# Kernel tuning notes

Hardware: AMD Instinct MI355X
Metric: run time of the kernel (lower is better)

The kernel has to match this reference:

```python
import jax, jax.numpy as jnp
import numpy as np

N_HEADS = 32
N_KV_HEADS = 8
HEAD_DIM = 128
ROPE_BASE = 10000.0
NEG_INF = -1e9


def rope(x, base=ROPE_BASE, offset=0):
    # x: [B, H, L, d]; 'traditional' RoPE with the module's rotation formula.
    d = x.shape[-1]
    t = jnp.arange(x.shape[2], dtype=jnp.float32) + offset
    freqs = base ** (-jnp.arange(0, d, 2, dtype=jnp.float32) / d)  # [d/2]
    ang = t[:, None] * freqs[None, :]                              # [L, d/2]
    cos, sin = jnp.cos(ang), jnp.sin(ang)
    x1, x2 = x[..., 0::2], x[..., 1::2]
    out = jnp.stack([x1 * cos + x2 * sin, x1 * sin - x2 * cos], axis=-1)
    return out.reshape(x.shape)


def setup_inputs() -> dict:
    key = jax.random.key(0)
    ks = jax.random.split(key, 5)
    B, L, D = 2, 2048, 4096
    x = jax.random.normal(ks[0], (B, L, D), dtype=jnp.float32)
    wq = jax.random.normal(ks[1], (D, N_HEADS * HEAD_DIM), dtype=jnp.float32) * 0.02
    wk = jax.random.normal(ks[2], (D, N_KV_HEADS * HEAD_DIM), dtype=jnp.float32) * 0.02
    wv = jax.random.normal(ks[3], (D, N_KV_HEADS * HEAD_DIM), dtype=jnp.float32) * 0.02
    wo = jax.random.normal(ks[4], (N_HEADS * HEAD_DIM, D), dtype=jnp.float32) * 0.02
    # causal additive mask [L, L]
    mask = jnp.where(jnp.tril(jnp.ones((L, L), dtype=bool)), 0.0, NEG_INF).astype(jnp.float32)
    return {"x": x, "mask": mask, "wq": wq, "wk": wk, "wv": wv, "wo": wo}


def reference(x, mask, wq, wk, wv, wo):
    B, L, D = x.shape
    scale = HEAD_DIM ** -0.5
    q = (x @ wq).reshape(B, L, N_HEADS, HEAD_DIM).transpose(0, 2, 1, 3)     # [B,H,L,d]
    k = (x @ wk).reshape(B, L, N_KV_HEADS, HEAD_DIM).transpose(0, 2, 1, 3)  # [B,Hk,L,d]
    v = (x @ wv).reshape(B, L, N_KV_HEADS, HEAD_DIM).transpose(0, 2, 1, 3)
    rep = N_HEADS // N_KV_HEADS
    k = jnp.repeat(k, rep, axis=1)  # [B,H,L,d]  (physical GQA repeat, as in source)
    v = jnp.repeat(v, rep, axis=1)
    q = rope(q)
    k = rope(k)
    scores = jnp.einsum("bhqd,bhkd->bhqk", q * scale, k) + mask  # [B,H,L,L]
    probs = jax.nn.softmax(scores.astype(jnp.float32), axis=-1).astype(scores.dtype)
    out = jnp.einsum("bhqk,bhkd->bhqd", probs, v)
    out = out.transpose(0, 2, 1, 3).reshape(B, L, N_HEADS * HEAD_DIM)
    return out @ wo, (k, v)
```

## Files before the change

### kernel.cpp

```cpp
#include <hip/hip_runtime.h>

typedef unsigned short u16;
typedef unsigned int u32;
typedef float f32x4 __attribute__((ext_vector_type(4)));
typedef __bf16 bf16x8 __attribute__((ext_vector_type(8)));

#define DEV __device__ __forceinline__

DEV u16 f2b(float f) {
    union { float f; u32 u; } v; v.f = f;
    u32 r = v.u + 0x7fffu + ((v.u >> 16) & 1u);
    return (u16)(r >> 16);
}
DEV float b2f(u16 b) {
    union { u32 u; float f; } v; v.u = ((u32)b) << 16;
    return v.f;
}

DEV void gload16(const void* g, void* l) {
    __builtin_amdgcn_global_load_lds((const __attribute__((address_space(1))) void*)g,
                                     (__attribute__((address_space(3))) void*)l, 16, 0, 0);
}

DEV f32x4 mfma16(bf16x8 a, bf16x8 b, f32x4 c) {
    return __builtin_amdgcn_mfma_f32_16x16x32_bf16(a, b, c, 0, 0, 0);
}

__global__ __launch_bounds__(256) void convx_kernel(const float* __restrict__ in,
                                                    u16* __restrict__ out) {
    size_t i = ((size_t)blockIdx.x * 256 + threadIdx.x) * 4;
    float4 v = *(const float4*)(in + i);
    ushort4 o; o.x = f2b(v.x); o.y = f2b(v.y); o.z = f2b(v.z); o.w = f2b(v.w);
    *(ushort4*)(out + i) = o;
}

__global__ __launch_bounds__(256) void tconv_kernel(const float* __restrict__ in,
                                                    u16* __restrict__ out, int K, int N) {
    __shared__ float tile[64][65];
    int t = threadIdx.x;
    int n0 = blockIdx.x * 64, k0 = blockIdx.y * 64;
    int r = t >> 4, c4 = (t & 15) * 4;
#pragma unroll
    for (int i = 0; i < 4; ++i) {
        float4 v = *(const float4*)(in + (size_t)(k0 + i * 16 + r) * N + n0 + c4);
        tile[i * 16 + r][c4 + 0] = v.x; tile[i * 16 + r][c4 + 1] = v.y;
        tile[i * 16 + r][c4 + 2] = v.z; tile[i * 16 + r][c4 + 3] = v.w;
    }
    __syncthreads();
#pragma unroll
    for (int i = 0; i < 4; ++i) {
        int nn = i * 16 + r;
        ushort4 o;
        o.x = f2b(tile[c4 + 0][nn]); o.y = f2b(tile[c4 + 1][nn]);
        o.z = f2b(tile[c4 + 2][nn]); o.w = f2b(tile[c4 + 3][nn]);
        *(ushort4*)(out + (size_t)(n0 + nn) * K + k0 + c4) = o;
    }
}

template <bool F32OUT>
__global__ __launch_bounds__(512, 2) void gemm256_kernel(const u16* __restrict__ A,
                                                         const u16* __restrict__ Bt,
                                                         u16* __restrict__ Cb,
                                                         float* __restrict__ Cf,
                                                         int M, int N, int K, int gy) {
    __shared__ __align__(16) u16 Asb[2][2][128 * 64];
    __shared__ __align__(16) u16 Bsb[2][2][128 * 64];
    (void)M;
    int t = threadIdx.x;
    int lane = t & 63, w = t >> 6;
    int wrM = w >> 2, wcN = w & 3;
    int lr = lane & 15, hi = lane >> 4;
    int wg = blockIdx.x;
    int swz = (wg & 7) * ((int)gridDim.x >> 3) + (wg >> 3);
    int bx = swz / gy, by = swz % gy;
    int m0 = by * 256, n0 = bx * 256;
    int nk = K >> 6;

    auto stageA = [&](int X, int h) {
        const u16* src = A + (size_t)(m0 + h * 128) * K + X * 64;
        char* dst = (char*)&Asb[X & 1][h][0];
#pragma unroll
        for (int it = 0; it < 2; ++it) {
            int c = it * 512 + t;
            int row = c >> 3;
            int col8 = ((c & 7) ^ (row & 7)) << 3;
            gload16(src + (size_t)row * K + col8, dst + (it * 512 + (t & ~63)) * 16);
        }
    };
    auto stageB = [&](int X, int h) {
        const u16* src = Bt + (size_t)(n0 + h * 128) * K + X * 64;
        char* dst = (char*)&Bsb[X & 1][h][0];
#pragma unroll
        for (int it = 0; it < 2; ++it) {
            int c = it * 512 + t;
            int row = c >> 3;
            int col8 = ((c & 7) ^ (row & 7)) << 3;
            gload16(src + (size_t)row * K + col8, dst + (it * 512 + (t & ~63)) * 16);
        }
    };

    stageA(0, 0); stageA(0, 1); stageB(0, 0); stageB(0, 1);
    stageA(1, 0); stageA(1, 1); stageB(1, 0);
    asm volatile("s_waitcnt vmcnt(6)" ::: "memory");
    __builtin_amdgcn_s_barrier();

    f32x4 acc[8][4] = {};
    for (int kt = 0; kt < nk; ++kt) {
        __builtin_amdgcn_sched_barrier(0);
        int p = kt & 1;
        const char* Ah = (const char*)&Asb[p][wrM][0];
        const char* Bh = (const char*)&Bsb[p][wcN >> 1][0];
        bool s1 = (kt + 1 < nk), s2 = (kt + 2 < nk);
        bf16x8 a[8][2], bb[2][2];

#pragma unroll
        for (int mf = 0; mf < 4; ++mf)
#pragma unroll
            for (int ks = 0; ks < 2; ++ks) {
                int row = mf * 16 + lr;
                int byt = (row * 128 + ks * 64 + hi * 16) ^ ((row & 7) << 4);
                a[mf][ks] = *(const bf16x8*)(Ah + byt);
            }
#pragma unroll
        for (int nf = 0; nf < 2; ++nf)
#pragma unroll
            for (int ks = 0; ks < 2; ++ks) {
                int row = (wcN & 1) * 64 + nf * 16 + lr;
                int byt = (row * 128 + ks * 64 + hi * 16) ^ ((row & 7) << 4);
                bb[nf][ks] = *(const bf16x8*)(Bh + byt);
            }
        if (s1) stageB(kt + 1, 1);
        __builtin_amdgcn_s_barrier();
        __builtin_amdgcn_s_setprio(1);
#pragma unroll
        for (int mf = 0; mf < 4; ++mf)
#pragma unroll
            for (int nf = 0; nf < 2; ++nf)
#pragma unroll
                for (int ks = 0; ks < 2; ++ks)
                    acc[mf][nf] = mfma16(a[mf][ks], bb[nf][ks], acc[mf][nf]);
        __builtin_amdgcn_s_setprio(0);
        __builtin_amdgcn_s_barrier();

#pragma unroll
        for (int mf = 4; mf < 8; ++mf)
#pragma unroll
            for (int ks = 0; ks < 2; ++ks) {
                int row = mf * 16 + lr;
                int byt = (row * 128 + ks * 64 + hi * 16) ^ ((row & 7) << 4);
                a[mf][ks] = *(const bf16x8*)(Ah + byt);
            }
        __builtin_amdgcn_s_barrier();
        __builtin_amdgcn_s_setprio(1);
#pragma unroll
        for (int mf = 4; mf < 8; ++mf)
#pragma unroll
            for (int nf = 0; nf < 2; ++nf)
#pragma unroll
                for (int ks = 0; ks < 2; ++ks)
                    acc[mf][nf] = mfma16(a[mf][ks], bb[nf][ks], acc[mf][nf]);
        __builtin_amdgcn_s_setprio(0);
        __builtin_amdgcn_s_barrier();

#pragma unroll
        for (int nf = 0; nf < 2; ++nf)
#pragma unroll
            for (int ks = 0; ks < 2; ++ks) {
                int row = (wcN & 1) * 64 + (nf + 2) * 16 + lr;
                int byt = (row * 128 + ks * 64 + hi * 16) ^ ((row & 7) << 4);
                bb[nf][ks] = *(const bf16x8*)(Bh + byt);
            }
        if (s2) { stageA(kt + 2, 0); stageA(kt + 2, 1); }
        __builtin_amdgcn_s_barrier();
        __builtin_amdgcn_s_setprio(1);
#pragma unroll
        for (int mf = 4; mf < 8; ++mf)
#pragma unroll
            for (int nf = 0; nf < 2; ++nf)
#pragma unroll
                for (int ks = 0; ks < 2; ++ks)
                    acc[mf][nf + 2] = mfma16(a[mf][ks], bb[nf][ks], acc[mf][nf + 2]);
        __builtin_amdgcn_s_setprio(0);
        __builtin_amdgcn_s_barrier();

        if (s2) stageB(kt + 2, 0);
        __builtin_amdgcn_s_barrier();
        __builtin_amdgcn_s_setprio(1);
#pragma unroll
        for (int mf = 0; mf < 4; ++mf)
#pragma unroll
            for (int nf = 0; nf < 2; ++nf)
#pragma unroll
                for (int ks = 0; ks < 2; ++ks)
                    acc[mf][nf + 2] = mfma16(a[mf][ks], bb[nf][ks], acc[mf][nf + 2]);
        __builtin_amdgcn_s_setprio(0);
        if (s1) {
            if (s2) asm volatile("s_waitcnt vmcnt(6)" ::: "memory");
            else    asm volatile("s_waitcnt vmcnt(0)" ::: "memory");
        }
        __builtin_amdgcn_s_barrier();
    }

#pragma unroll
    for (int mf = 0; mf < 8; ++mf)
#pragma unroll
        for (int nf = 0; nf < 4; ++nf)
#pragma unroll
            for (int r = 0; r < 4; ++r) {
                int m = m0 + wrM * 128 + mf * 16 + hi * 4 + r;
                int n = n0 + wcN * 64 + nf * 16 + lr;
                if (F32OUT) Cf[(size_t)m * N + n] = acc[mf][nf][r];
                else        Cb[(size_t)m * N + n] = f2b(acc[mf][nf][r]);
            }
}

__global__ __launch_bounds__(256) void rope_kernel(u16* __restrict__ qkv,
                                                   float* __restrict__ outk) {
    int row = blockIdx.y;
    int p = blockIdx.x * 256 + threadIdx.x;
    int b = row >> 11, l = row & 2047;
    float freq = exp2f((float)(p & 63) * -0.2076205059304601f);
    float sv, cv; sincosf((float)l * freq, &sv, &cv);
    if (p < 2048) {
        int h = p >> 6, i = p & 63;
        size_t idx = (size_t)row * 6144 + h * 128 + 2 * i;
        u32 pr = *(const u32*)(qkv + idx);
        float x1 = b2f((u16)(pr & 0xffff)), x2 = b2f((u16)(pr >> 16));
        float o1 = x1 * cv + x2 * sv, o2 = x1 * sv - x2 * cv;
        *(u32*)(qkv + idx) = (u32)f2b(o1) | ((u32)f2b(o2) << 16);
    } else {
        int kvh = (p >> 6) - 32, i = p & 63;
        size_t idx = (size_t)row * 6144 + 4096 + kvh * 128 + 2 * i;
        u32 pr = *(const u32*)(qkv + idx);
        float x1 = b2f((u16)(pr & 0xffff)), x2 = b2f((u16)(pr >> 16));
        float o1 = x1 * cv + x2 * sv, o2 = x1 * sv - x2 * cv;
        *(u32*)(qkv + idx) = (u32)f2b(o1) | ((u32)f2b(o2) << 16);
#pragma unroll
        for (int r = 0; r < 4; ++r) {
            float2 o; o.x = o1; o.y = o2;
            *(float2*)(outk + ((size_t)((b * 32 + kvh * 4 + r) * 2048) + l) * 128 + 2 * i) = o;
        }
    }
}

__global__ __launch_bounds__(256) void vtrans_kernel(const u16* __restrict__ qkv,
                                                     u16* __restrict__ vt,
                                                     float* __restrict__ outv) {
    __shared__ u16 tile[64][65];
    int t = threadIdx.x;
    int l0 = blockIdx.x * 64, d0 = blockIdx.y * 64;
    int z = blockIdx.z, b = z >> 3, kvh = z & 7;
    int r = t >> 4, c4 = (t & 15) * 4;
#pragma unroll
    for (int i = 0; i < 4; ++i) {
        int l = l0 + i * 16 + r;
        ushort4 v = *(const ushort4*)(qkv + (size_t)(b * 2048 + l) * 6144 + 5120 + kvh * 128 + d0 + c4);
        tile[i * 16 + r][c4 + 0] = v.x; tile[i * 16 + r][c4 + 1] = v.y;
        tile[i * 16 + r][c4 + 2] = v.z; tile[i * 16 + r][c4 + 3] = v.w;
        float4 f; f.x = b2f(v.x); f.y = b2f(v.y); f.z = b2f(v.z); f.w = b2f(v.w);
#pragma unroll
        for (int rr = 0; rr < 4; ++rr)
            *(float4*)(outv + ((size_t)((b * 32 + kvh * 4 + rr) * 2048) + l) * 128 + d0 + c4) = f;
    }
    __syncthreads();
#pragma unroll
    for (int i = 0; i < 4; ++i) {
        int dn = i * 16 + r;
        ushort4 o;
        o.x = tile[c4 + 0][dn]; o.y = tile[c4 + 1][dn];
        o.z = tile[c4 + 2][dn]; o.w = tile[c4 + 3][dn];
        *(ushort4*)(vt + (size_t)((b * 8 + kvh) * 128 + d0 + dn) * 2048 + l0 + c4) = o;
    }
}

__global__ __launch_bounds__(256) void attn_kernel(const u16* __restrict__ qkv,
                                                   const u16* __restrict__ vt,
                                                   u16* __restrict__ ab) {
    __shared__ __align__(16) u16 Kbuf[2][64 * 128];
    __shared__ __align__(16) u16 Vbuf[2][128 * 64];
    __shared__ __align__(16) u16 Ps[4][16 * 64];
    int t = threadIdx.x, lane = t & 63, w = t >> 6;
    int lr = lane & 15, hi = lane >> 4;
    int h = blockIdx.y, b = blockIdx.z, kvh = h >> 2;

    const u16* kbase = qkv + (size_t)(b * 2048) * 6144 + 4096 + kvh * 128;
    const u16* vtbase = vt + (size_t)((b * 8 + kvh) * 128) * 2048;

    auto stageKV = [&](int k0, int buf) {
#pragma unroll
        for (int i = 0; i < 4; ++i) {
            int c = i * 256 + t;
            int row = c >> 4;
            int col8 = ((c & 15) ^ (row & 7)) << 3;
            gload16(kbase + (size_t)(k0 + row) * 6144 + col8,
                    (char*)Kbuf[buf] + (i * 256 + (t & ~63)) * 16);
        }
#pragma unroll
        for (int i = 0; i < 4; ++i) {
            int c = i * 256 + t;
            int row = c >> 3;
            int col8 = ((c & 7) ^ (row & 7)) << 3;
            gload16(vtbase + (size_t)row * 2048 + k0 + col8,
                    (char*)Vbuf[buf] + (i * 256 + (t & ~63)) * 16);
        }
    };

    auto process = [&](int qblk) {
        int q0 = qblk * 64;
        int qr = w * 16 + lr;
        bf16x8 qf[4];
#pragma unroll
        for (int kki = 0; kki < 4; ++kki)
            qf[kki] = *(const bf16x8*)(qkv + (size_t)(b * 2048 + q0 + qr) * 6144 + h * 128 +
                                       kki * 32 + 8 * hi);
        f32x4 acc[8] = {};
        float mrun[4], lrun[4];
#pragma unroll
        for (int r = 0; r < 4; ++r) { mrun[r] = -1e30f; lrun[r] = 0.f; }

        int nt = qblk + 1;
        stageKV(0, 0);
        __syncthreads();
        int cur = 0;
        for (int kt = 0; kt < nt; ++kt) {
            if (kt + 1 < nt) stageKV((kt + 1) * 64, cur ^ 1);
            __builtin_amdgcn_sched_barrier(0);

            const u16* Ks = Kbuf[cur];
            const u16* Vs = Vbuf[cur];
            f32x4 s[4] = {};
            __builtin_amdgcn_s_setprio(1);
#pragma unroll
            for (int kki = 0; kki < 4; ++kki) {
                bf16x8 kf[4];
#pragma unroll
                for (int fc = 0; fc < 4; ++fc) {
                    int kvr = fc * 16 + lr;
                    int byt = (kvr * 256 + (kki * 32 + 8 * hi) * 2) ^ ((kvr & 7) << 4);
                    kf[fc] = *(const bf16x8*)((const char*)Ks + byt);
                }
#pragma unroll
                for (int fc = 0; fc < 4; ++fc) s[fc] = mfma16(qf[kki], kf[fc], s[fc]);
            }
            __builtin_amdgcn_s_setprio(0);
            const float SC = 0.08838834764831845f;
            int diag = (kt == nt - 1);
#pragma unroll
            for (int fc = 0; fc < 4; ++fc)
#pragma unroll
                for (int r = 0; r < 4; ++r) {
                    float v = s[fc][r] * SC;
                    if (diag && (fc * 16 + lr) > (w * 16 + hi * 4 + r)) v = -1e30f;
                    s[fc][r] = v;
                }
            float fr[4];
#pragma unroll
            for (int r = 0; r < 4; ++r) {
                float v = fmaxf(fmaxf(s[0][r], s[1][r]), fmaxf(s[2][r], s[3][r]));
                v = fmaxf(v, __shfl_xor(v, 1)); v = fmaxf(v, __shfl_xor(v, 2));
                v = fmaxf(v, __shfl_xor(v, 4)); v = fmaxf(v, __shfl_xor(v, 8));
                float mn = fmaxf(mrun[r], v);
                fr[r] = __expf(mrun[r] - mn);
                mrun[r] = mn;
            }
#pragma unroll
            for (int fc = 0; fc < 4; ++fc)
#pragma unroll
                for (int r = 0; r < 4; ++r) s[fc][r] = __expf(s[fc][r] - mrun[r]);
#pragma unroll
            for (int r = 0; r < 4; ++r) {
                float v = s[0][r] + s[1][r] + s[2][r] + s[3][r];
                v += __shfl_xor(v, 1); v += __shfl_xor(v, 2);
                v += __shfl_xor(v, 4); v += __shfl_xor(v, 8);
                lrun[r] = lrun[r] * fr[r] + v;
            }
#pragma unroll
            for (int dhf = 0; dhf < 8; ++dhf)
#pragma unroll
                for (int r = 0; r < 4; ++r) acc[dhf][r] *= fr[r];
            u16* Pw = Ps[w];
#pragma unroll
            for (int fc = 0; fc < 4; ++fc)
#pragma unroll
                for (int r = 0; r < 4; ++r) {
                    int prow = hi * 4 + r, pcol = fc * 16 + lr;
                    int byt = (prow * 128 + pcol * 2) ^ ((prow & 7) << 4);
                    *(u16*)((char*)Pw + byt) = f2b(s[fc][r]);
                }
            asm volatile("s_waitcnt lgkmcnt(0)" ::: "memory");
            __builtin_amdgcn_s_setprio(1);
#pragma unroll
            for (int kk2 = 0; kk2 < 2; ++kk2) {
                int bytp = (lr * 128 + (kk2 * 32 + 8 * hi) * 2) ^ ((lr & 7) << 4);
                bf16x8 pf = *(const bf16x8*)((const char*)Pw + bytp);
#pragma unroll
                for (int dhf = 0; dhf < 8; ++dhf) {
                    int dh = dhf * 16 + lr;
                    int bytv = (dh * 128 + (kk2 * 32 + 8 * hi) * 2) ^ ((dh & 7) << 4);
                    bf16x8 vf = *(const bf16x8*)((const char*)Vs + bytv);
                    acc[dhf] = mfma16(pf, vf, acc[dhf]);
                }
            }
            __builtin_amdgcn_s_setprio(0);
            __syncthreads();
            cur ^= 1;
        }
#pragma unroll
        for (int dhf = 0; dhf < 8; ++dhf)
#pragma unroll
            for (int r = 0; r < 4; ++r) {
                int qrow = q0 + w * 16 + hi * 4 + r;
                int dh = dhf * 16 + lr;
                ab[(size_t)(b * 2048 + qrow) * 4096 + h * 128 + dh] = f2b(acc[dhf][r] / lrun[r]);
            }
    };

    process(31 - blockIdx.x);
    __syncthreads();
    process(blockIdx.x);
}

extern "C" void kernel_launch(void* const* d_in, const int* in_sizes, int n_in,
                              void* d_out, int out_size, void* d_ws, size_t ws_size,
                              hipStream_t stream) {
    (void)in_sizes; (void)n_in; (void)out_size; (void)ws_size;
    const float* x  = (const float*)d_in[0];
    const float* wq = (const float*)d_in[2];
    const float* wk = (const float*)d_in[3];
    const float* wv = (const float*)d_in[4];
    const float* wo = (const float*)d_in[5];

    char* ws = (char*)d_ws;
    u16* xb  = (u16*)(ws + 0);
    u16* fBt = (u16*)(ws + 33554432);
    u16* qkv = (u16*)(ws + 83886080);
    u16* vt  = (u16*)(ws + 134217728);
    u16* ab  = xb;
    u16* wob = fBt;

    float* out0 = (float*)d_out;
    float* outk = out0 + 16777216;
    float* outv = out0 + 33554432;

    convx_kernel<<<16384, 256, 0, stream>>>(x, xb);
    tconv_kernel<<<dim3(64, 64), 256, 0, stream>>>(wq, fBt, 4096, 4096);
    tconv_kernel<<<dim3(16, 64), 256, 0, stream>>>(wk, fBt + (size_t)4096 * 4096, 4096, 1024);
    tconv_kernel<<<dim3(16, 64), 256, 0, stream>>>(wv, fBt + (size_t)5120 * 4096, 4096, 1024);

    gemm256_kernel<false><<<384, 512, 0, stream>>>(xb, fBt, qkv, nullptr, 4096, 6144, 4096, 16);

    tconv_kernel<<<dim3(64, 64), 256, 0, stream>>>(wo, wob, 4096, 4096);

    rope_kernel<<<dim3(10, 4096), 256, 0, stream>>>(qkv, outk);
    vtrans_kernel<<<dim3(32, 2, 16), 256, 0, stream>>>(qkv, vt, outv);

    attn_kernel<<<dim3(16, 32, 2), 256, 0, stream>>>(qkv, vt, ab);

    gemm256_kernel<true><<<256, 512, 0, stream>>>(ab, wob, nullptr, out0, 4096, 4096, 4096, 16);
}
```

Before: 653.7 us.

## Use 256x192 tile GEMM for QKV projection to fill all CUs

Adds a new GEMM kernel with 256x192 output tiles for the fused QKV projection, launching 512 workgroups instead of 384 with 256x256 tiles. With 256 CUs, 384 tiles leave a partial second wave, while 512 tiles divide evenly. The kernel reorders loads and MFMA phases so the third N-fragment loads and the staging of the next stages interleave with compute. Launch bounds on the existing 256 kernel also change to one block per SM, which may alter register allocation for the output projection.

```diff
diff --git a/kernel.cpp b/kernel.cpp
--- a/kernel.cpp
+++ b/kernel.cpp
@@ -57,8 +57,153 @@
     }
 }
 
+__global__ __launch_bounds__(512, 1) void gemm192_kernel(const u16* __restrict__ A,
+                                                         const u16* __restrict__ Bt,
+                                                         u16* __restrict__ Cb,
+                                                         int N, int K, int gy) {
+    __shared__ __align__(16) u16 Asb[2][2][128 * 64];
+    __shared__ __align__(16) u16 Bsb[2][192 * 64];
+    int t = threadIdx.x;
+    int lane = t & 63, w = t >> 6;
+    int wrM = w >> 2, wcN = w & 3;
+    int lr = lane & 15, hi = lane >> 4;
+    int wg = blockIdx.x;
+    int swz = (wg & 7) * ((int)gridDim.x >> 3) + (wg >> 3);
+    int bx = swz / gy, by = swz % gy;
+    int m0 = by * 256, n0 = bx * 192;
+    int nk = K >> 6;
+
+    auto stageA = [&](int X) {
+        const u16* src = A + (size_t)m0 * K + X * 64;
+        char* dst = (char*)&Asb[X & 1][0][0];
+#pragma unroll
+        for (int it = 0; it < 4; ++it) {
+            int c = it * 512 + t;
+            int row = c >> 3;
+            int col8 = ((c & 7) ^ (row & 7)) << 3;
+            gload16(src + (size_t)row * K + col8, dst + (it * 512 + (t & ~63)) * 16);
+        }
+    };
+    auto stageB = [&](int X) {
+        const u16* src = Bt + (size_t)n0 * K + X * 64;
+        char* dst = (char*)&Bsb[X & 1][0];
+#pragma unroll
+        for (int it = 0; it < 3; ++it) {
+            int c = it * 512 + t;
+            int row = c >> 3;
+            int col8 = ((c & 7) ^ (row & 7)) << 3;
+            gload16(src + (size_t)row * K + col8, dst + (it * 512 + (t & ~63)) * 16);
+        }
+    };
+
+    stageA(0); stageB(0); stageA(1); stageB(1);
+    asm volatile("s_waitcnt vmcnt(7)" ::: "memory");
+    __builtin_amdgcn_s_barrier();
+
+    f32x4 acc[8][3] = {};
+    for (int kt = 0; kt < nk; ++kt) {
+        __builtin_amdgcn_sched_barrier(0);
+        int p = kt & 1;
+        const char* Ah = (const char*)&Asb[p][wrM][0];
+        const char* Bh = (const char*)&Bsb[p][0];
+        bool s1 = (kt + 1 < nk), s2 = (kt + 2 < nk);
+        bf16x8 a[8][2], bb[2][2], bc[2];
+
+#pragma unroll
+        for (int mf = 0; mf < 4; ++mf)
+#pragma unroll
+            for (int ks = 0; ks < 2; ++ks) {
+                int row = mf * 16 + lr;
+                int byt = (row * 128 + ks * 64 + hi * 16) ^ ((row & 7) << 4);
+                a[mf][ks] = *(const bf16x8*)(Ah + byt);
+            }
+#pragma unroll
+        for (int nf = 0; nf < 2; ++nf)
+#pragma unroll
+            for (int ks = 0; ks < 2; ++ks) {
+                int row = wcN * 48 + nf * 16 + lr;
+                int byt = (row * 128 + ks * 64 + hi * 16) ^ ((row & 7) << 4);
+                bb[nf][ks] = *(const bf16x8*)(Bh + byt);
+            }
+        __builtin_amdgcn_s_barrier();
+        __builtin_amdgcn_s_setprio(1);
+#pragma unroll
+        for (int mf = 0; mf < 4; ++mf)
+#pragma unroll
+            for (int nf = 0; nf < 2; ++nf)
+#pragma unroll
+                for (int ks = 0; ks < 2; ++ks)
+                    acc[mf][nf] = mfma16(a[mf][ks], bb[nf][ks], acc[mf][nf]);
+        __builtin_amdgcn_s_setprio(0);
+        __builtin_amdgcn_s_barrier();
+
+#pragma unroll
+        for (int mf = 4; mf < 8; ++mf)
+#pragma unroll
+            for (int ks = 0; ks < 2; ++ks) {
+                int row = mf * 16 + lr;
+                int byt = (row * 128 + ks * 64 + hi * 16) ^ ((row & 7) << 4);
+                a[mf][ks] = *(const bf16x8*)(Ah + byt);
+            }
+        __builtin_amdgcn_s_barrier();
+        __builtin_amdgcn_s_setprio(1);
+#pragma unroll
+        for (int mf = 4; mf < 8; ++mf)
+#pragma unroll
+            for (int nf = 0; nf < 2; ++nf)
+#pragma unroll
+                for (int ks = 0; ks < 2; ++ks)
+                    acc[mf][nf] = mfma16(a[mf][ks], bb[nf][ks], acc[mf][nf]);
+        __builtin_amdgcn_s_setprio(0);
+        __builtin_amdgcn_s_barrier();
+
+#pragma unroll
+        for (int ks = 0; ks < 2; ++ks) {
+            int row = wcN * 48 + 32 + lr;
+            int byt = (row * 128 + ks * 64 + hi * 16) ^ ((row & 7) << 4);
+            bc[ks] = *(const bf16x8*)(Bh + byt);
+        }
+        if (s2) stageA(kt + 2);
+        __builtin_amdgcn_s_barrier();
+        __builtin_amdgcn_s_setprio(1);
+#pragma unroll
+        for (int mf = 4; mf < 8; ++mf)
+#pragma unroll
+            for (int ks = 0; ks < 2; ++ks)
+                acc[mf][2] = mfma16(a[mf][ks], bc[ks], acc[mf][2]);
+        __builtin_amdgcn_s_setprio(0);
+        __builtin_amdgcn_s_barrier();
+
+        if (s2) stageB(kt + 2);
+        __builtin_amdgcn_s_barrier();
+        __builtin_amdgcn_s_setprio(1);
+#pragma unroll
+        for (int mf = 0; mf < 4; ++mf)
+#pragma unroll
+            for (int ks = 0; ks < 2; ++ks)
+                acc[mf][2] = mfma16(a[mf][ks], bc[ks], acc[mf][2]);
+        __builtin_amdgcn_s_setprio(0);
+        if (s1) {
+            if (s2) asm volatile("s_waitcnt vmcnt(7)" ::: "memory");
+            else    asm volatile("s_waitcnt vmcnt(0)" ::: "memory");
+        }
+        __builtin_amdgcn_s_barrier();
+    }
+
+#pragma unroll
+    for (int mf = 0; mf < 8; ++mf)
+#pragma unroll
+        for (int nf = 0; nf < 3; ++nf)
+#pragma unroll
+            for (int r = 0; r < 4; ++r) {
+                int m = m0 + wrM * 128 + mf * 16 + hi * 4 + r;
+                int n = n0 + wcN * 48 + nf * 16 + lr;
+                Cb[(size_t)m * N + n] = f2b(acc[mf][nf][r]);
+            }
+}
+
 template <bool F32OUT>
-__global__ __launch_bounds__(512, 2) void gemm256_kernel(const u16* __restrict__ A,
+__global__ __launch_bounds__(512, 1) void gemm256_kernel(const u16* __restrict__ A,
                                                          const u16* __restrict__ Bt,
                                                          u16* __restrict__ Cb,
                                                          float* __restrict__ Cf,
@@ -447,7 +592,7 @@
     tconv_kernel<<<dim3(16, 64), 256, 0, stream>>>(wk, fBt + (size_t)4096 * 4096, 4096, 1024);
     tconv_kernel<<<dim3(16, 64), 256, 0, stream>>>(wv, fBt + (size_t)5120 * 4096, 4096, 1024);
 
-    gemm256_kernel<false><<<384, 512, 0, stream>>>(xb, fBt, qkv, nullptr, 4096, 6144, 4096, 16);
+    gemm192_kernel<<<512, 512, 0, stream>>>(xb, fBt, qkv, 6144, 4096, 16);
 
     tconv_kernel<<<dim3(64, 64), 256, 0, stream>>>(wo, wob, 4096, 4096);
 
```

New measurement: 650.8 us. Within noise of the previous version (-0.4%).

## Reschedule GEMM prefetch to one-ahead B, two-ahead A with 2x unrolled k-loop

Applied to the files above, without the earlier changes.

Restructures the GEMM main-loop prefetch schedule so B tiles are loaded one iteration ahead and A tiles two ahead, spreading the four half-tile loads evenly across the four MFMA phases. The wait count and the prologue are adjusted to match. The k-loop is manually unrolled by two so the LDS buffer index is a compile-time constant. The schedule now relies on B for tile kt+1 landing within a single iteration, which could expose load latency, and it assumes nk is even. The unused M parameter is also removed.

```diff
diff --git a/kernel.cpp b/kernel.cpp
--- a/kernel.cpp
+++ b/kernel.cpp
@@ -62,10 +62,9 @@
                                                          const u16* __restrict__ Bt,
                                                          u16* __restrict__ Cb,
                                                          float* __restrict__ Cf,
-                                                         int M, int N, int K, int gy) {
+                                                         int N, int K, int gy) {
     __shared__ __align__(16) u16 Asb[2][2][128 * 64];
     __shared__ __align__(16) u16 Bsb[2][2][128 * 64];
-    (void)M;
     int t = threadIdx.x;
     int lane = t & 63, w = t >> 6;
     int wrM = w >> 2, wcN = w & 3;
@@ -100,17 +99,16 @@
     };
 
     stageA(0, 0); stageA(0, 1); stageB(0, 0); stageB(0, 1);
-    stageA(1, 0); stageA(1, 1); stageB(1, 0);
-    asm volatile("s_waitcnt vmcnt(6)" ::: "memory");
+    stageA(1, 0); stageA(1, 1);
+    asm volatile("s_waitcnt vmcnt(4)" ::: "memory");
     __builtin_amdgcn_s_barrier();
 
     f32x4 acc[8][4] = {};
-    for (int kt = 0; kt < nk; ++kt) {
-        __builtin_amdgcn_sched_barrier(0);
-        int p = kt & 1;
+
+    auto tile = [&](int kt, int p) __attribute__((always_inline)) {
         const char* Ah = (const char*)&Asb[p][wrM][0];
         const char* Bh = (const char*)&Bsb[p][wcN >> 1][0];
-        bool s1 = (kt + 1 < nk), s2 = (kt + 2 < nk);
+        bool sB = (kt + 1 < nk), sA = (kt + 2 < nk);
         bf16x8 a[8][2], bb[2][2];
 
 #pragma unroll
@@ -118,18 +116,16 @@
 #pragma unroll
             for (int ks = 0; ks < 2; ++ks) {
                 int row = mf * 16 + lr;
-                int byt = (row * 128 + ks * 64 + hi * 16) ^ ((row & 7) << 4);
-                a[mf][ks] = *(const bf16x8*)(Ah + byt);
+                a[mf][ks] = *(const bf16x8*)(Ah + ((row * 128 + ks * 64 + hi * 16) ^ ((row & 7) << 4)));
             }
 #pragma unroll
         for (int nf = 0; nf < 2; ++nf)
 #pragma unroll
             for (int ks = 0; ks < 2; ++ks) {
                 int row = (wcN & 1) * 64 + nf * 16 + lr;
-                int byt = (row * 128 + ks * 64 + hi * 16) ^ ((row & 7) << 4);
-                bb[nf][ks] = *(const bf16x8*)(Bh + byt);
-            }
-        if (s1) stageB(kt + 1, 1);
+                bb[nf][ks] = *(const bf16x8*)(Bh + ((row * 128 + ks * 64 + hi * 16) ^ ((row & 7) << 4)));
+            }
+        if (sB) stageB(kt + 1, 0);
         __builtin_amdgcn_s_barrier();
         __builtin_amdgcn_s_setprio(1);
 #pragma unroll
@@ -147,9 +143,9 @@
 #pragma unroll
             for (int ks = 0; ks < 2; ++ks) {
                 int row = mf * 16 + lr;
-                int byt = (row * 128 + ks * 64 + hi * 16) ^ ((row & 7) << 4);
-                a[mf][ks] = *(const bf16x8*)(Ah + byt);
-            }
+                a[mf][ks] = *(const bf16x8*)(Ah + ((row * 128 + ks * 64 + hi * 16) ^ ((row & 7) << 4)));
+            }
+        if (sB) stageB(kt + 1, 1);
         __builtin_amdgcn_s_barrier();
         __builtin_amdgcn_s_setprio(1);
 #pragma unroll
@@ -167,10 +163,9 @@
 #pragma unroll
             for (int ks = 0; ks < 2; ++ks) {
                 int row = (wcN & 1) * 64 + (nf + 2) * 16 + lr;
-                int byt = (row * 128 + ks * 64 + hi * 16) ^ ((row & 7) << 4);
-                bb[nf][ks] = *(const bf16x8*)(Bh + byt);
-            }
-        if (s2) { stageA(kt + 2, 0); stageA(kt + 2, 1); }
+                bb[nf][ks] = *(const bf16x8*)(Bh + ((row * 128 + ks * 64 + hi * 16) ^ ((row & 7) << 4)));
+            }
+        if (sA) stageA(kt + 2, 0);
         __builtin_amdgcn_s_barrier();
         __builtin_amdgcn_s_setprio(1);
 #pragma unroll
@@ -183,7 +178,7 @@
         __builtin_amdgcn_s_setprio(0);
         __builtin_amdgcn_s_barrier();
 
-        if (s2) stageB(kt + 2, 0);
+        if (sA) stageA(kt + 2, 1);
         __builtin_amdgcn_s_barrier();
         __builtin_amdgcn_s_setprio(1);
 #pragma unroll
@@ -194,11 +189,14 @@
                 for (int ks = 0; ks < 2; ++ks)
                     acc[mf][nf + 2] = mfma16(a[mf][ks], bb[nf][ks], acc[mf][nf + 2]);
         __builtin_amdgcn_s_setprio(0);
-        if (s1) {
-            if (s2) asm volatile("s_waitcnt vmcnt(6)" ::: "memory");
-            else    asm volatile("s_waitcnt vmcnt(0)" ::: "memory");
-        }
-        __builtin_amdgcn_s_barrier();
+        if (sA)      asm volatile("s_waitcnt vmcnt(4)" ::: "memory");
+        else if (sB) asm volatile("s_waitcnt vmcnt(0)" ::: "memory");
+        __builtin_amdgcn_s_barrier();
+    };
+
+    for (int kt = 0; kt < nk; kt += 2) {
+        tile(kt, 0);
+        tile(kt + 1, 1);
     }
 
 #pragma unroll
@@ -447,7 +445,7 @@
     tconv_kernel<<<dim3(16, 64), 256, 0, stream>>>(wk, fBt + (size_t)4096 * 4096, 4096, 1024);
     tconv_kernel<<<dim3(16, 64), 256, 0, stream>>>(wv, fBt + (size_t)5120 * 4096, 4096, 1024);
 
-    gemm256_kernel<false><<<384, 512, 0, stream>>>(xb, fBt, qkv, nullptr, 4096, 6144, 4096, 16);
+    gemm256_kernel<false><<<384, 512, 0, stream>>>(xb, fBt, qkv, nullptr, 6144, 4096, 16);
 
     tconv_kernel<<<dim3(64, 64), 256, 0, stream>>>(wo, wob, 4096, 4096);
 
@@ -456,5 +454,5 @@
 
     attn_kernel<<<dim3(16, 32, 2), 256, 0, stream>>>(qkv, vt, ab);
 
-    gemm256_kernel<true><<<256, 512, 0, stream>>>(ab, wob, nullptr, out0, 4096, 4096, 4096, 16);
-}
+    gemm256_kernel<true><<<256, 512, 0, stream>>>(ab, wob, nullptr, out0, 4096, 4096, 16);
+}
```

New measurement: 704.4 us. 1.08x slower.
